# Optimization experiments

Measured on AMD Instinct MI355X. Metric: run time of the kernel, lower is better.

## Reference

```python
import jax, jax.numpy as jnp
import numpy as np

B, N, F, T = 8, 4096, 3, 12
D = 64            # model_dim
AH, DK, DV = 4, 32, 32   # attention headers, k_dim, v_dim
GH = 8            # gat_headers == out_features
E = 524288


def _ln(x, g, b, eps=1e-5):
    m = jnp.mean(x, -1, keepdims=True)
    v = jnp.mean((x - m) ** 2, -1, keepdims=True)
    return (x - m) * jax.lax.rsqrt(v + eps) * g + b


def _glu(x, w, b, C):
    # x: [B, C, N, L], w: [2C, C, 1, k] -> causal-style valid conv + SiLU gate
    y = jax.lax.conv_general_dilated(x, w, (1, 1), 'VALID',
                                     dimension_numbers=('NCHW', 'OIHW', 'NCHW'))
    y = y + b[None, :, None, None]
    return jax.nn.silu(y[:, :C]) * y[:, C:]


def setup_inputs():
    key = jax.random.key(0)
    ks = jax.random.split(key, 20)
    s = jnp.float32(0.02)
    return {
        'data': jax.random.normal(ks[0], (B, N, F, T), jnp.float32),
        'edges': jax.random.randint(ks[1], (2, E), 0, B * N),
        'embT_w': jax.random.normal(ks[2], (T, N)) * s,
        'embT_g': jnp.ones((N,)), 'embT_b': jnp.zeros((N,)),
        'wq': jax.random.normal(ks[3], (N, AH * DK)) * s,
        'wk': jax.random.normal(ks[4], (N, AH * DK)) * s,
        'wv': jax.random.normal(ks[5], (N, AH * DV)) * s,
        'wo': jax.random.normal(ks[6], (AH * DV, N)) * s,
        'tat_g': jnp.ones((N,)), 'tat_b': jnp.zeros((N,)),
        'mix_w': jax.random.normal(ks[7], (D, T, F)) * s,
        'mix_b': jnp.zeros((D,)),
        'embS_w': jax.random.normal(ks[8], (N, D)) * s,
        'embS_g': jnp.ones((D,)), 'embS_b': jnp.zeros((D,)),
        'gat_wl': jax.random.normal(ks[9], (D, GH * T)) * s,
        'gat_bl': jnp.zeros((GH * T,)),
        'gat_wr': jax.random.normal(ks[10], (D, GH * T)) * s,
        'gat_br': jnp.zeros((GH * T,)),
        'gat_att': jax.random.normal(ks[11], (GH, T)) * s,
        'gat_bias': jnp.zeros((GH * T,)),
        'g3_w': jax.random.normal(ks[12], (2 * GH, GH, 1, 3)) * s, 'g3_b': jnp.zeros((2 * GH,)),
        'g5_w': jax.random.normal(ks[13], (2 * GH, GH, 1, 5)) * s, 'g5_b': jnp.zeros((2 * GH,)),
        'g7_w': jax.random.normal(ks[14], (2 * GH, GH, 1, 7)) * s, 'g7_b': jnp.zeros((2 * GH,)),
        'fc_w': jax.random.normal(ks[15], (3 * T - 12, T)) * s, 'fc_b': jnp.zeros((T,)),
        'res_w': jax.random.normal(ks[16], (GH, F)) * s, 'res_b': jnp.zeros((GH,)),
        'ln_g': jnp.ones((GH,)), 'ln_b': jnp.zeros((GH,)),
    }


def reference(data, edges, embT_w, embT_g, embT_b, wq, wk, wv, wo, tat_g, tat_b,
              mix_w, mix_b, embS_w, embS_g, embS_b,
              gat_wl, gat_bl, gat_wr, gat_br, gat_att, gat_bias,
              g3_w, g3_b, g5_w, g5_b, g7_w, g7_b, fc_w, fc_b,
              res_w, res_b, ln_g, ln_b):
    # ---- EmbedT: [B,N,F,T] -> [B,F,T,N] plus learned temporal positional table
    x = data.transpose(0, 2, 3, 1) + embT_w[None, None]
    x = _ln(x, embT_g, embT_b)

    # ---- Temporal MHA over T (model_dim = N), dropout = identity in eval
    resid = x
    q = (x @ wq).reshape(B, F, T, AH, DK)
    k = (x @ wk).reshape(B, F, T, AH, DK)
    v = (x @ wv).reshape(B, F, T, AH, DV)
    scores = jnp.einsum('bfqhd,bfkhd->bfhqk', q, k) / jnp.sqrt(jnp.float32(DK))
    attn = jax.nn.softmax(scores, axis=-1)
    ctx = jnp.einsum('bfhqk,bfkhd->bfqhd', attn, v).reshape(B, F, T, AH * DV)
    x = _ln(ctx @ wo + resid, tat_g, tat_b)

    # ---- feature_temporal_mixer: Conv2d(T, D, (1, F)) on [B,T,N,F] -> [B,N,D]
    x = jnp.einsum('bftn,dtf->bnd', x, mix_w) + mix_b

    # ---- EmbedS
    x = _ln(x + embS_w[None], embS_g, embS_b)

    # ---- GATv2Conv over B*N nodes (add_self_loops=True, leaky slope 0.2)
    BN = B * N
    xf = x.reshape(BN, D)
    xl = (xf @ gat_wl + gat_bl).reshape(BN, GH, T)
    xr = (xf @ gat_wr + gat_br).reshape(BN, GH, T)
    loop = jnp.arange(BN)
    src = jnp.concatenate([edges[0], loop])
    dst = jnp.concatenate([edges[1], loop])
    feat = jax.nn.leaky_relu(xl[src] + xr[dst], 0.2)          # [E+BN, GH, T]
    e = jnp.einsum('eht,ht->eh', feat, gat_att)
    m = jax.ops.segment_max(e, dst, num_segments=BN)
    ex = jnp.exp(e - m[dst])
    ssum = jax.ops.segment_sum(ex, dst, num_segments=BN)
    alpha = ex / ssum[dst]
    out = jax.ops.segment_sum(xl[src] * alpha[:, :, None], dst, num_segments=BN)
    out = out.reshape(BN, GH * T) + gat_bias

    res_gate = out.reshape(B, N, GH, T).transpose(0, 2, 1, 3)  # [B,GH,N,T]

    # ---- gated convs (GLU) kernels 3/5/7 -> concat -> fc
    g = jnp.concatenate([_glu(res_gate, g3_w, g3_b, GH),
                         _glu(res_gate, g5_w, g5_b, GH),
                         _glu(res_gate, g7_w, g7_b, GH)], axis=-1)  # [B,GH,N,3T-12]
    x = jax.nn.relu(g @ fc_w + fc_b)   # features_num == 3 branch

    # ---- residual 1x1 conv over feature channels of raw data
    x_res = jnp.einsum('bfnt,of->bont', data.transpose(0, 2, 1, 3), res_w) \
            + res_b[None, :, None, None]
    x = jax.nn.relu(x_res + x)         # [B,GH,N,T]
    x = _ln(x.transpose(0, 3, 2, 1), ln_g, ln_b)  # LN over GH on [B,T,N,GH]
    return x.transpose(0, 2, 3, 1)     # [B,N,GH,T]
```

## Files before the change

### kernel.cpp

```cpp
#include <hip/hip_runtime.h>
#include <hip/hip_bf16.h>

typedef __hip_bfloat16 bf16;
typedef short bf16x8 __attribute__((ext_vector_type(8)));
typedef float f32x4 __attribute__((ext_vector_type(4)));
typedef unsigned short u16x4 __attribute__((ext_vector_type(4)));

constexpr int B = 8, N = 4096, F = 3, T = 12;
constexpr int Dm = 64, AH = 4, DK = 32;
constexpr int GH = 8;
constexpr int E = 524288;
constexpr int BN = B * N;
constexpr int ROWS = B * F * T;
constexpr int HD = AH * DK;
constexpr int PSZ = ROWS * 384;
constexpr int KSPLIT = 8;

__device__ __forceinline__ float b2f(bf16 x) { return __bfloat162float(x); }
__device__ __forceinline__ float u2f(unsigned short u) {
  return __uint_as_float(((unsigned)u) << 16);
}

constexpr unsigned C_EMBTW=0, C_EMBTG=49152, C_EMBTB=53248, C_WQ=57344,
  C_WK=581632, C_WV=1105920, C_WO=1630208, C_TATG=2154496, C_TATB=2158592,
  C_MIXW=2162688, C_MIXB=2164992, C_EMBSW=2165056, C_EMBSG=2427200,
  C_EMBSB=2427264, C_GWL=2427328, C_GBL=2433472, C_GWR=2433568,
  C_GBR=2439712, C_GATT=2439808, C_GBIAS=2439904, C_G3W=2440000,
  C_G3B=2440384, C_G5W=2440400, C_G5B=2441040, C_G7W=2441056,
  C_G7B=2441952, C_FCW=2441968, C_FCB=2442256, C_RW=2442268, C_RB=2442292,
  C_LNG=2442300, C_LNB=2442308, C_TOT=2442316;

__device__ const unsigned CUM[33] = {
  0,49152,53248,57344,581632,1105920,1630208,2154496,2158592,2162688,
  2164992,2165056,2427200,2427264,2427328,2433472,2433568,2439712,2439808,
  2439904,2440000,2440384,2440400,2441040,2441056,2441952,2441968,2442256,
  2442268,2442292,2442300,2442308,2442316};

constexpr size_t OFF_CVT = 16;
constexpr size_t OFF_X1  = OFF_CVT + 2442320;
constexpr size_t OFF_CTXB= OFF_X1  + (size_t)ROWS * N;
constexpr size_t OFF_X2  = OFF_CTXB+ (size_t)ROWS * HD;
constexpr size_t OFF_X3  = OFF_X2  + (size_t)ROWS * N;
constexpr size_t OFF_XL  = OFF_X3  + (size_t)BN * Dm;
constexpr size_t OFF_XR  = OFF_XL  + (size_t)BN * GH * T / 2;
constexpr size_t OFF_RG  = OFF_XR  + (size_t)BN * GH * T / 2;
constexpr size_t OFF_INT = OFF_RG  + (size_t)BN * GH * T;
constexpr size_t OFF_X2R = OFF_INT + 600000;
constexpr size_t OFF_WT16 = OFF_RG;
constexpr size_t OFF_WO16 = OFF_RG + 786432;
constexpr size_t OFF_X1B  = OFF_RG + 786432 + 262144;
constexpr size_t OFF_PP   = OFF_X1B + 294912;
constexpr size_t OFF_WOT  = OFF_PP + (size_t)KSPLIT * PSZ;
constexpr size_t OFF_GWT  = OFF_WOT + 262144;

struct Srcs { const void* p[32]; };
__global__ __launch_bounds__(256) void k_convert(
    const unsigned* __restrict__ g1, Srcs s, float* __restrict__ dst,
    bf16* __restrict__ wo16, int* __restrict__ cnt) {
  int f = (g1[0] != 0x3F800000u);
  for (unsigned gid = blockIdx.x * 256 + threadIdx.x;
       gid < C_TOT + 524288u + (unsigned)BN; gid += gridDim.x * 256) {
    if (gid < C_TOT) {
      int lo = 0, hi = 31;
      while (lo < hi) { int mid = (lo + hi + 1) >> 1; if (gid >= CUM[mid]) lo = mid; else hi = mid - 1; }
      if (lo >= 3 && lo <= 5) continue;
      unsigned off = gid - CUM[lo];
      dst[gid] = f ? b2f(((const bf16*)s.p[lo])[off]) : ((const float*)s.p[lo])[off];
    } else if (gid < C_TOT + 524288u) {
      unsigned off = gid - C_TOT;
      wo16[off] = f ? ((const bf16*)s.p[6])[off]
                    : __float2bfloat16(((const float*)s.p[6])[off]);
    } else {
      cnt[gid - C_TOT - 524288u] = 0;
    }
  }
}

__global__ __launch_bounds__(256) void k_wtrans(
    const unsigned* __restrict__ g1, const void* __restrict__ wq,
    const void* __restrict__ wk, const void* __restrict__ wv,
    bf16* __restrict__ wt) {
  __shared__ float t[32][33];
  int fl = (g1[0] != 0x3F800000u);
  int bid = blockIdx.x;
  int tc = bid / 128, tk = bid - tc * 128;
  int k0 = tk * 32, c0 = tc * 32;
  int mat = c0 >> 7, cloc = c0 & 127;
  const void* src = (mat == 0) ? wq : ((mat == 1) ? wk : wv);
  int tid = threadIdx.x;
  int r = tid >> 5, cc = tid & 31;
#pragma unroll
  for (int p = 0; p < 4; p++) {
    int row = p * 8 + r;
    size_t idx = (size_t)(k0 + row) * 128 + cloc + cc;
    t[row][cc] = fl ? b2f(((const bf16*)src)[idx]) : ((const float*)src)[idx];
  }
  __syncthreads();
#pragma unroll
  for (int p = 0; p < 4; p++) {
    int crow = p * 8 + r;
    wt[(size_t)(c0 + crow) * 4096 + k0 + cc] = __float2bfloat16(t[cc][crow]);
  }
}

__global__ __launch_bounds__(256) void k_wotrans(
    const bf16* __restrict__ wo, bf16* __restrict__ wot) {
  __shared__ bf16 t[32][33];
  int bid = blockIdx.x;
  int tn = bid >> 2, tk = bid & 3;
  int n0 = tn * 32, k0 = tk * 32;
  int tid = threadIdx.x;
  int r = tid >> 5, cc = tid & 31;
#pragma unroll
  for (int p = 0; p < 4; p++) {
    int row = p * 8 + r;
    t[row][cc] = wo[(size_t)(k0 + row) * 4096 + n0 + cc];
  }
  __syncthreads();
#pragma unroll
  for (int p = 0; p < 4; p++) {
    int crow = p * 8 + r;
    wot[(size_t)(n0 + crow) * 128 + k0 + cc] = t[cc][crow];
  }
}

__global__ __launch_bounds__(256) void k_gat_w(
    const float* __restrict__ wl, const float* __restrict__ wr,
    bf16* __restrict__ wlrt) {
  int idx = blockIdx.x * 256 + threadIdx.x;
  if (idx >= 192 * 64) return;
  int c = idx >> 6, k = idx & 63;
  float v = (c < 96) ? wl[(size_t)k * 96 + c] : wr[(size_t)k * 96 + (c - 96)];
  wlrt[idx] = __float2bfloat16(v);
}

__global__ __launch_bounds__(1024) void k_embt_ln(
    const unsigned* __restrict__ g1, const void* __restrict__ data,
    const float* __restrict__ w, const float* __restrict__ g,
    const float* __restrict__ b_, float* __restrict__ x1,
    bf16* __restrict__ x1b) {
  __shared__ float red[32];
  int row = blockIdx.x;
  int t = row % T; int bf_ = row / T; int f = bf_ % F; int bb = bf_ / F;
  int tid = threadIdx.x;
  int fl = (g1[0] != 0x3F800000u);
  float dv[4];
  if (fl) {
#pragma unroll
    for (int i = 0; i < 4; i++) {
      int n = i * 1024 + tid;
      dv[i] = b2f(((const bf16*)data)[(size_t)(bb * N + n) * 36 + f * 12 + t]);
    }
  } else {
#pragma unroll
    for (int i = 0; i < 4; i++) {
      int n = i * 1024 + tid;
      dv[i] = ((const float*)data)[(size_t)(bb * N + n) * 36 + f * 12 + t];
    }
  }
  float vals[4]; float s = 0.f, s2 = 0.f;
#pragma unroll
  for (int i = 0; i < 4; i++) {
    int n = i * 1024 + tid;
    float v = dv[i] + w[t * N + n];
    vals[i] = v; s += v; s2 += v * v;
  }
#pragma unroll
  for (int o = 32; o > 0; o >>= 1) { s += __shfl_down(s, o, 64); s2 += __shfl_down(s2, o, 64); }
  int lane = tid & 63, wid = tid >> 6;
  if (lane == 0) { red[wid] = s; red[16 + wid] = s2; }
  __syncthreads();
  float S = 0.f, S2 = 0.f;
#pragma unroll
  for (int j = 0; j < 16; j++) { S += red[j]; S2 += red[16 + j]; }
  float mean = S / (float)N;
  float var = S2 / (float)N - mean * mean;
  float inv = rsqrtf(var + 1e-5f);
#pragma unroll
  for (int i = 0; i < 4; i++) {
    int n = i * 1024 + tid;
    float o = (vals[i] - mean) * inv * g[n] + b_[n];
    x1[(size_t)row * N + n] = o;
    x1b[(size_t)row * N + n] = __float2bfloat16(o);
  }
}

__global__ __launch_bounds__(256) void k_qkv_mma(
    const bf16* __restrict__ x1b, const bf16* __restrict__ wt,
    float* __restrict__ pp) {
  int wave = (blockIdx.x * 256 + threadIdx.x) >> 6;
  int lane = threadIdx.x & 63;
  int ks = wave & 7, tile = wave >> 3;
  int mt = tile / 24, nt = tile - mt * 24;
  int m = lane & 15, quad = lane >> 4;
  const bf16* ap = x1b + (size_t)(mt * 16 + m) * 4096 + ks * 512 + quad * 8;
  const bf16* bp = wt  + (size_t)(nt * 16 + m) * 4096 + ks * 512 + quad * 8;
  f32x4 acc = {0.f, 0.f, 0.f, 0.f};
  for (int kk = 0; kk < 512; kk += 32) {
    bf16x8 a = *(const bf16x8*)(ap + kk);
    bf16x8 b = *(const bf16x8*)(bp + kk);
    acc = __builtin_amdgcn_mfma_f32_16x16x32_bf16(a, b, acc, 0, 0, 0);
  }
  float* o = pp + ((size_t)ks * ROWS + mt * 16 + quad * 4) * 384 + nt * 16 + m;
#pragma unroll
  for (int r = 0; r < 4; r++) o[(size_t)r * 384] = acc[r];
}

__global__ __launch_bounds__(64) void k_attn(
    const float* __restrict__ pp, bf16* __restrict__ ctxb) {
  int blk = blockIdx.x; int h = blk & 3; int bf_ = blk >> 2;
  int tid = threadIdx.x;
  __shared__ float qs[12][32], ks[12][32], vs[12][32], att[12][12];
  for (int idx = tid; idx < 384; idx += 64) {
    int t = idx >> 5, d = idx & 31;
    int base = (bf_ * T + t) * 384 + h * 32 + d;
    float qv = 0.f, kv = 0.f, vv = 0.f;
#pragma unroll
    for (int p = 0; p < KSPLIT; p++) {
      qv += pp[(size_t)p * PSZ + base];
      kv += pp[(size_t)p * PSZ + base + 128];
      vv += pp[(size_t)p * PSZ + base + 256];
    }
    qs[t][d] = qv; ks[t][d] = kv; vs[t][d] = vv;
  }
  __syncthreads();
  for (int idx = tid; idx < 144; idx += 64) {
    int qt = idx / 12, kt = idx - qt * 12;
    float s = 0.f;
#pragma unroll
    for (int d = 0; d < 32; d++) s += qs[qt][d] * ks[kt][d];
    att[qt][kt] = s * 0.1767766953f;
  }
  __syncthreads();
  if (tid < 12) {
    float m = -1e30f;
#pragma unroll
    for (int j = 0; j < 12; j++) m = fmaxf(m, att[tid][j]);
    float ss = 0.f;
#pragma unroll
    for (int j = 0; j < 12; j++) { float e = __expf(att[tid][j] - m); att[tid][j] = e; ss += e; }
    float inv = 1.f / ss;
#pragma unroll
    for (int j = 0; j < 12; j++) att[tid][j] *= inv;
  }
  __syncthreads();
  for (int idx = tid; idx < 384; idx += 64) {
    int t = idx >> 5, d = idx & 31;
    float s = 0.f;
#pragma unroll
    for (int j = 0; j < 12; j++) s += att[t][j] * vs[j][d];
    ctxb[(size_t)(bf_ * T + t) * HD + h * 32 + d] = __float2bfloat16(s);
  }
}

__global__ __launch_bounds__(256) void k_proj_mma(
    const bf16* __restrict__ ctxb, const bf16* __restrict__ wot,
    const float* __restrict__ x1, float* __restrict__ x2r) {
  int wave = (blockIdx.x * 256 + threadIdx.x) >> 6;
  int lane = threadIdx.x & 63;
  int nt = wave & 255, mt = wave >> 8;
  int m = lane & 15, quad = lane >> 4;
  const bf16* ap = ctxb + (size_t)(mt * 16 + m) * 128 + quad * 8;
  const bf16* bp = wot  + (size_t)(nt * 16 + m) * 128 + quad * 8;
  f32x4 acc = {0.f, 0.f, 0.f, 0.f};
#pragma unroll
  for (int kk = 0; kk < 128; kk += 32) {
    bf16x8 a = *(const bf16x8*)(ap + kk);
    bf16x8 b = *(const bf16x8*)(bp + kk);
    acc = __builtin_amdgcn_mfma_f32_16x16x32_bf16(a, b, acc, 0, 0, 0);
  }
  int row0 = mt * 16 + quad * 4, col = nt * 16 + m;
#pragma unroll
  for (int r = 0; r < 4; r++) {
    size_t idx = (size_t)(row0 + r) * N + col;
    x2r[idx] = acc[r] + x1[idx];
  }
}

__global__ __launch_bounds__(1024) void k_ln2(
    const float* __restrict__ x2r, const float* __restrict__ g,
    const float* __restrict__ b_, float* __restrict__ x2) {
  __shared__ float red[32];
  int row = blockIdx.x, tid = threadIdx.x;
  float vals[4]; float s = 0.f, s2 = 0.f;
#pragma unroll
  for (int i = 0; i < 4; i++) {
    int n = i * 1024 + tid;
    float v = x2r[(size_t)row * N + n];
    vals[i] = v; s += v; s2 += v * v;
  }
#pragma unroll
  for (int o = 32; o > 0; o >>= 1) { s += __shfl_down(s, o, 64); s2 += __shfl_down(s2, o, 64); }
  int lane = tid & 63, wid = tid >> 6;
  if (lane == 0) { red[wid] = s; red[16 + wid] = s2; }
  __syncthreads();
  float S = 0.f, S2 = 0.f;
#pragma unroll
  for (int j = 0; j < 16; j++) { S += red[j]; S2 += red[16 + j]; }
  float mean = S / (float)N;
  float var = S2 / (float)N - mean * mean;
  float inv = rsqrtf(var + 1e-5f);
#pragma unroll
  for (int i = 0; i < 4; i++) {
    int n = i * 1024 + tid;
    x2[(size_t)row * N + n] = (vals[i] - mean) * inv * g[n] + b_[n];
  }
}

__global__ __launch_bounds__(256) void k_mix_ln(
    const float* __restrict__ x2, const float* __restrict__ mw,
    const float* __restrict__ mb, const float* __restrict__ sw,
    const float* __restrict__ g, const float* __restrict__ b_,
    bf16* __restrict__ x3b) {
  int tid = threadIdx.x; int wid = tid >> 6; int d = tid & 63;
  int ng = blockIdx.x * 4 + wid;
  int bb = ng >> 12; int n = ng & (N - 1);
  float acc = mb[d];
#pragma unroll
  for (int t = 0; t < T; t++)
#pragma unroll
    for (int f = 0; f < F; f++)
      acc += x2[((size_t)(bb * F + f) * T + t) * N + n] * mw[(d * T + t) * F + f];
  acc += sw[(size_t)n * Dm + d];
  float s = acc, s2 = acc * acc;
#pragma unroll
  for (int m = 1; m < 64; m <<= 1) { s += __shfl_xor(s, m, 64); s2 += __shfl_xor(s2, m, 64); }
  float mean = s * (1.f / 64.f), var = s2 * (1.f / 64.f) - mean * mean;
  float inv = rsqrtf(var + 1e-5f);
  x3b[(size_t)ng * Dm + d] = __float2bfloat16((acc - mean) * inv * g[d] + b_[d]);
}

__global__ __launch_bounds__(256) void k_gat_mma(
    const bf16* __restrict__ x3b, const bf16* __restrict__ wlrt,
    const float* __restrict__ bl, const float* __restrict__ br,
    bf16* __restrict__ xl, bf16* __restrict__ xr) {
  __shared__ __align__(16) bf16 bs[192 * 64];
  int tid = threadIdx.x;
  {
    const bf16x8* src = (const bf16x8*)wlrt;
    bf16x8* dst = (bf16x8*)bs;
#pragma unroll
    for (int i = 0; i < 6; i++) {
      int ci = i * 256 + tid;
      dst[ci ^ ((ci >> 3) & 7)] = src[ci];
    }
  }
  __syncthreads();
  int wave = tid >> 6, lane = tid & 63;
  int mt = blockIdx.x * 4 + wave;
  int m = lane & 15, quad = lane >> 4;
  const bf16* ap = x3b + (size_t)(mt * 16 + m) * 64 + quad * 8;
  bf16x8 a0 = *(const bf16x8*)(ap);
  bf16x8 a1 = *(const bf16x8*)(ap + 32);
  const bf16x8* bs8 = (const bf16x8*)bs;
  int row0 = mt * 16 + quad * 4;
#pragma unroll
  for (int nt = 0; nt < 12; nt++) {
    int r = nt * 16 + m;
    int c0 = r * 8 + quad;
    bf16x8 b0 = bs8[c0 ^ (r & 7)];
    bf16x8 b1 = bs8[(c0 + 4) ^ (r & 7)];
    f32x4 acc = {0.f, 0.f, 0.f, 0.f};
    acc = __builtin_amdgcn_mfma_f32_16x16x32_bf16(a0, b0, acc, 0, 0, 0);
    acc = __builtin_amdgcn_mfma_f32_16x16x32_bf16(a1, b1, acc, 0, 0, 0);
    bool left = r < 96;
    int c = left ? r : r - 96;
    float bias = left ? bl[c] : br[c];
    bf16* o = left ? xl : xr;
#pragma unroll
    for (int rr = 0; rr < 4; rr++)
      o[(size_t)(row0 + rr) * 96 + c] = __float2bfloat16(acc[rr] + bias);
  }
}

__global__ __launch_bounds__(256) void k_hist(
    const int* __restrict__ edges, int* __restrict__ cnt) {
  int e = blockIdx.x * 256 + threadIdx.x;
  if (e < E) atomicAdd(cnt + edges[E + e], 1);
}

__global__ __launch_bounds__(1024) void k_scan(
    const int* __restrict__ cnt, int* __restrict__ off, int* __restrict__ cur) {
  __shared__ int part[1024];
  int tid = threadIdx.x;
  int base = tid * 32;
  int local[32]; int s = 0;
#pragma unroll
  for (int j = 0; j < 32; j++) { local[j] = cnt[base + j]; s += local[j]; }
  part[tid] = s;
  __syncthreads();
  for (int d = 1; d < 1024; d <<= 1) {
    int v = (tid >= d) ? part[tid - d] : 0;
    __syncthreads();
    part[tid] += v;
    __syncthreads();
  }
  int run = part[tid] - s;
#pragma unroll
  for (int j = 0; j < 32; j++) {
    off[base + j] = run; cur[base + j] = run;
    run += local[j];
  }
  if (tid == 1023) off[BN] = E;
}

__global__ __launch_bounds__(256) void k_scatter(
    const int* __restrict__ edges, int* __restrict__ cur, int* __restrict__ srcs) {
  int e = blockIdx.x * 256 + threadIdx.x;
  if (e < E) {
    int pos = atomicAdd(cur + edges[E + e], 1);
    srcs[pos] = edges[e];
  }
}

__device__ __forceinline__ void ld12bf(const bf16* p, float* l) {
  u16x4 a = *(const u16x4*)p;
  u16x4 b = *(const u16x4*)(p + 4);
  u16x4 c = *(const u16x4*)(p + 8);
  l[0]=u2f(a.x); l[1]=u2f(a.y); l[2]=u2f(a.z); l[3]=u2f(a.w);
  l[4]=u2f(b.x); l[5]=u2f(b.y); l[6]=u2f(b.z); l[7]=u2f(b.w);
  l[8]=u2f(c.x); l[9]=u2f(c.y); l[10]=u2f(c.z); l[11]=u2f(c.w);
}

__global__ __launch_bounds__(256) void k_gat(
    const int* __restrict__ off, const int* __restrict__ srcs,
    const bf16* __restrict__ xl, const bf16* __restrict__ xr,
    const float* __restrict__ att, const float* __restrict__ bias,
    float* __restrict__ rg) {
  int tid = threadIdx.x;
  int wv = tid >> 6, lane = tid & 63;
  int es = lane >> 3, h = lane & 7;
  int dst = blockIdx.x * 4 + wv;
  int bb = dst >> 12, n = dst & (N - 1);
  size_t rbase = (size_t)dst * 96 + h * 12;
  float xd[12], at[12];
  ld12bf(xr + rbase, xd);
#pragma unroll
  for (int t = 0; t < 12; t++) at[t] = att[h * 12 + t];

  float acc[12];
#pragma unroll
  for (int t = 0; t < 12; t++) acc[t] = 0.f;
  float ssum = 0.f;
  if (es == 0) {
    float l[12];
    ld12bf(xl + rbase, l);
    float sc = 0.f;
#pragma unroll
    for (int t = 0; t < 12; t++) {
      float sv = l[t] + xd[t];
      float fr = sv > 0.f ? sv : 0.2f * sv;
      sc += fr * at[t];
    }
    float ex = __expf(sc);
    ssum = ex;
#pragma unroll
    for (int t = 0; t < 12; t++) acc[t] = l[t] * ex;
  }
  int st = off[dst], en = off[dst + 1];
  for (int j = st + es; j < en; j += 8) {
    int src = srcs[j];
    float l[12];
    ld12bf(xl + (size_t)src * 96 + h * 12, l);
    float sc = 0.f;
#pragma unroll
    for (int t = 0; t < 12; t++) {
      float sv = l[t] + xd[t];
      float fr = sv > 0.f ? sv : 0.2f * sv;
      sc += fr * at[t];
    }
    float ex = __expf(sc);
    ssum += ex;
#pragma unroll
    for (int t = 0; t < 12; t++) acc[t] += l[t] * ex;
  }
#pragma unroll
  for (int m = 8; m < 64; m <<= 1) {
    ssum += __shfl_xor(ssum, m, 64);
#pragma unroll
    for (int t = 0; t < 12; t++) acc[t] += __shfl_xor(acc[t], m, 64);
  }
  if (es == 0) {
    float inv = 1.f / ssum;
    float* op = rg + ((size_t)(bb * 8 + h) * N + n) * 12;
#pragma unroll
    for (int t = 0; t < 12; t++)
      op[t] = acc[t] * inv + bias[h * 12 + t];
  }
}

__global__ __launch_bounds__(768) void k_tail(
    const unsigned* __restrict__ g1, const float* __restrict__ rg,
    const float* __restrict__ g3w, const float* __restrict__ g3b,
    const float* __restrict__ g5w, const float* __restrict__ g5b,
    const float* __restrict__ g7w, const float* __restrict__ g7b,
    const float* __restrict__ fcw, const float* __restrict__ fcb,
    const void* __restrict__ data, const float* __restrict__ rw,
    const float* __restrict__ rb, const float* __restrict__ lng,
    const float* __restrict__ lnb, void* __restrict__ out) {
  int tid = threadIdx.x;
  int br = tid >> 8;
  int u = tid & 255;
  int h = u & 7, i = u >> 3;
  int blk = blockIdx.x;
  int bb = blk >> 7;
  int n0 = (blk & 127) * 32;
  int n = n0 + i;
  int fl = (g1[0] != 0x3F800000u);
  __shared__ float xs[32][100];
  __shared__ float dds[32][40];
  __shared__ float wpk[8 * 260 + 4];
  __shared__ float fcs[288];
  __shared__ float gbuf[24][256];
  __shared__ float b3s[16], b5s[16], b7s[16], fcbs[12], lngs[8], lnbs[8], rws[24], rbs[8];
  for (int idx = tid; idx < 3072; idx += 768) {
    int c = idx / 384; int within = idx - c * 384;
    int ii = within / 12, t = within - ii * 12;
    xs[ii][c * 12 + t] = rg[((size_t)(bb * 8 + c) * N + n0 + ii) * 12 + t];
  }
  if (fl) {
    for (int idx = tid; idx < 1152; idx += 768) {
      int nn = idx / 36, jj = idx - nn * 36;
      dds[nn][jj] = b2f(((const bf16*)data)[(size_t)(bb * N + n0 + nn) * 36 + jj]);
    }
  } else {
    for (int idx = tid; idx < 1152; idx += 768) {
      int nn = idx / 36, jj = idx - nn * 36;
      dds[nn][jj] = ((const float*)data)[(size_t)(bb * N + n0 + nn) * 36 + jj];
    }
  }
  for (int idx = tid; idx < 1920; idx += 768) {
    int hh = idx / 240; int r = idx - hh * 240; int c = r / 30; int tap = r - c * 30;
    float v;
    if (tap < 3)       v = g3w[hh * 24 + c * 3 + tap];
    else if (tap < 6)  v = g3w[(hh + 8) * 24 + c * 3 + (tap - 3)];
    else if (tap < 11) v = g5w[hh * 40 + c * 5 + (tap - 6)];
    else if (tap < 16) v = g5w[(hh + 8) * 40 + c * 5 + (tap - 11)];
    else if (tap < 23) v = g7w[hh * 56 + c * 7 + (tap - 16)];
    else               v = g7w[(hh + 8) * 56 + c * 7 + (tap - 23)];
    wpk[hh * 260 + c * 32 + tap] = v;
  }
  for (int idx = tid; idx < 288; idx += 768) fcs[idx] = fcw[idx];
  if (tid < 16) { b3s[tid] = g3b[tid]; b5s[tid] = g5b[tid]; b7s[tid] = g7b[tid]; }
  if (tid < 12) fcbs[tid] = fcb[tid];
  if (tid < 24) rws[tid] = rw[tid];
  if (tid < 8) { lngs[tid] = lng[tid]; lnbs[tid] = lnb[tid]; rbs[tid] = rb[tid]; }
  __syncthreads();
  const float* x = xs[i];
  const float* wbase = &wpk[h * 260];
  if (br == 0) {
    float pa[10], pb[10];
    float ba = b3s[h], bbv = b3s[h + 8];
#pragma unroll
    for (int l = 0; l < 10; l++) { pa[l] = ba; pb[l] = bbv; }
#pragma unroll
    for (int c = 0; c < 8; c++) {
      float4 xa = *(const float4*)&x[c * 12];
      float4 xb = *(const float4*)&x[c * 12 + 4];
      float4 xc = *(const float4*)&x[c * 12 + 8];
      float xr[12] = {xa.x, xa.y, xa.z, xa.w, xb.x, xb.y, xb.z, xb.w,
                      xc.x, xc.y, xc.z, xc.w};
      const float* wpc = wbase + c * 32;
      float4 wA = *(const float4*)wpc;
      float2 wB = *(const float2*)(wpc + 4);
#pragma unroll
      for (int l = 0; l < 10; l++) {
        pa[l] += xr[l] * wA.x + xr[l + 1] * wA.y + xr[l + 2] * wA.z;
        pb[l] += xr[l] * wA.w + xr[l + 1] * wB.x + xr[l + 2] * wB.y;
      }
    }
#pragma unroll
    for (int l = 0; l < 10; l++)
      gbuf[l][u] = pa[l] / (1.f + __expf(-pa[l])) * pb[l];
  } else if (br == 1) {
    float pa[8], pb[8];
    float ba = b5s[h], bbv = b5s[h + 8];
#pragma unroll
    for (int l = 0; l < 8; l++) { pa[l] = ba; pb[l] = bbv; }
#pragma unroll
    for (int c = 0; c < 8; c++) {
      float4 xa = *(const float4*)&x[c * 12];
      float4 xb = *(const float4*)&x[c * 12 + 4];
      float4 xc = *(const float4*)&x[c * 12 + 8];
      float xr[12] = {xa.x, xa.y, xa.z, xa.w, xb.x, xb.y, xb.z, xb.w,
                      xc.x, xc.y, xc.z, xc.w};
      const float* wpc = wbase + c * 32;
      float2 w0 = *(const float2*)(wpc + 6);
      float2 w1 = *(const float2*)(wpc + 8);
      float2 w2 = *(const float2*)(wpc + 10);
      float2 w3 = *(const float2*)(wpc + 12);
      float2 w4 = *(const float2*)(wpc + 14);
      float wt[10] = {w0.x, w0.y, w1.x, w1.y, w2.x, w2.y, w3.x, w3.y, w4.x, w4.y};
#pragma unroll
      for (int l = 0; l < 8; l++) {
        float a = 0.f, bsum = 0.f;
#pragma unroll
        for (int j = 0; j < 5; j++) { a += xr[l + j] * wt[j]; bsum += xr[l + j] * wt[5 + j]; }
        pa[l] += a; pb[l] += bsum;
      }
    }
#pragma unroll
    for (int l = 0; l < 8; l++)
      gbuf[10 + l][u] = pa[l] / (1.f + __expf(-pa[l])) * pb[l];
  } else {
    float pa[6], pb[6];
    float ba = b7s[h], bbv = b7s[h + 8];
#pragma unroll
    for (int l = 0; l < 6; l++) { pa[l] = ba; pb[l] = bbv; }
#pragma unroll
    for (int c = 0; c < 8; c++) {
      float4 xa = *(const float4*)&x[c * 12];
      float4 xb = *(const float4*)&x[c * 12 + 4];
      float4 xc = *(const float4*)&x[c * 12 + 8];
      float xr[12] = {xa.x, xa.y, xa.z, xa.w, xb.x, xb.y, xb.z, xb.w,
                      xc.x, xc.y, xc.z, xc.w};
      const float* wpc = wbase + c * 32;
      float4 wA = *(const float4*)(wpc + 16);
      float4 wB = *(const float4*)(wpc + 20);
      float4 wC = *(const float4*)(wpc + 24);
      float2 wD = *(const float2*)(wpc + 28);
      float wt[14] = {wA.x, wA.y, wA.z, wA.w, wB.x, wB.y, wB.z, wB.w,
                      wC.x, wC.y, wC.z, wC.w, wD.x, wD.y};
#pragma unroll
      for (int l = 0; l < 6; l++) {
        float a = 0.f, bsum = 0.f;
#pragma unroll
        for (int j = 0; j < 7; j++) { a += xr[l + j] * wt[j]; bsum += xr[l + j] * wt[7 + j]; }
        pa[l] += a; pb[l] += bsum;
      }
    }
#pragma unroll
    for (int l = 0; l < 6; l++)
      gbuf[18 + l][u] = pa[l] / (1.f + __expf(-pa[l])) * pb[l];
  }
  __syncthreads();
  if (br == 0) {
    float gv[24];
#pragma unroll
    for (int l = 0; l < 24; l++) gv[l] = gbuf[l][u];
    float rw0 = rws[h * 3 + 0], rw1 = rws[h * 3 + 1], rw2 = rws[h * 3 + 2], rb0 = rbs[h];
    size_t obase = ((size_t)(bb * N + n) * GH + h) * T;
#pragma unroll
    for (int t = 0; t < 12; t++) {
      float a = fcbs[t];
#pragma unroll
      for (int l = 0; l < 24; l++) a += gv[l] * fcs[l * 12 + t];
      a = fmaxf(a, 0.f);
      float r = rb0 + dds[i][t] * rw0 + dds[i][12 + t] * rw1 + dds[i][24 + t] * rw2;
      float v = fmaxf(a + r, 0.f);
      float s = v, s2 = v * v;
#pragma unroll
      for (int m = 1; m < 8; m <<= 1) { s += __shfl_xor(s, m, 64); s2 += __shfl_xor(s2, m, 64); }
      float mean = s * 0.125f, var = s2 * 0.125f - mean * mean;
      float inv = rsqrtf(var + 1e-5f);
      float o = (v - mean) * inv * lngs[h] + lnbs[h];
      if (fl) ((bf16*)out)[obase + t] = __float2bfloat16(o);
      else    ((float*)out)[obase + t] = o;
    }
  }
}

extern "C" void kernel_launch(void* const* d_in, const int* in_sizes, int n_in,
                              void* d_out, int out_size, void* d_ws, size_t ws_size,
                              hipStream_t stream) {
  const void* data  = d_in[0];
  const int*  edges = (const int*)d_in[1];
  const unsigned* g1 = (const unsigned*)d_in[3];

  float* ws = (float*)d_ws;
  float* cv  = ws + OFF_CVT;
  float* x1  = ws + OFF_X1;  float* x2 = ws + OFF_X2;
  float* x2r = ws + OFF_X2R;
  bf16* x3b  = (bf16*)(ws + OFF_X3);
  bf16* ctxb = (bf16*)(ws + OFF_CTXB);
  bf16* xl   = (bf16*)(ws + OFF_XL);
  bf16* xr   = (bf16*)(ws + OFF_XR);
  float* rg  = ws + OFF_RG;
  bf16* wt16 = (bf16*)(ws + OFF_WT16);
  bf16* wo16 = (bf16*)(ws + OFF_WO16);
  bf16* x1b  = (bf16*)(ws + OFF_X1B);
  bf16* wot16= (bf16*)(ws + OFF_WOT);
  bf16* wlrt = (bf16*)(ws + OFF_GWT);
  float* pp  = ws + OFF_PP;
  int* ibase = (int*)(ws + OFF_INT);
  int* cnt  = ibase;
  int* off  = ibase + BN;
  int* srcs = ibase + 2 * BN + 16;

  Srcs s;
  for (int i = 0; i < 32; i++) s.p[i] = d_in[2 + i];

  k_convert<<<2048, 256, 0, stream>>>(g1, s, cv, wo16, cnt);
  k_wtrans<<<12 * 128, 256, 0, stream>>>(g1, d_in[5], d_in[6], d_in[7], wt16);
  k_wotrans<<<512, 256, 0, stream>>>(wo16, wot16);
  k_gat_w<<<48, 256, 0, stream>>>(cv + C_GWL, cv + C_GWR, wlrt);
  k_embt_ln<<<ROWS, 1024, 0, stream>>>(g1, data, cv + C_EMBTW, cv + C_EMBTG,
                                       cv + C_EMBTB, x1, x1b);
  k_qkv_mma<<<864, 256, 0, stream>>>(x1b, wt16, pp);
  k_attn<<<B * F * AH, 64, 0, stream>>>(pp, ctxb);
  k_proj_mma<<<1152, 256, 0, stream>>>(ctxb, wot16, x1, x2r);
  k_ln2<<<ROWS, 1024, 0, stream>>>(x2r, cv + C_TATG, cv + C_TATB, x2);
  k_mix_ln<<<BN / 4, 256, 0, stream>>>(x2, cv + C_MIXW, cv + C_MIXB, cv + C_EMBSW,
                                       cv + C_EMBSG, cv + C_EMBSB, x3b);
  k_gat_mma<<<512, 256, 0, stream>>>(x3b, wlrt, cv + C_GBL, cv + C_GBR, xl, xr);
  k_hist<<<E / 256, 256, 0, stream>>>(edges, cnt);
  k_scan<<<1, 1024, 0, stream>>>(cnt, off, cnt);
  k_scatter<<<E / 256, 256, 0, stream>>>(edges, cnt, srcs);
  k_gat<<<BN / 4, 256, 0, stream>>>(off, srcs, xl, xr, cv + C_GATT, cv + C_GBIAS, rg);
  k_tail<<<BN / 32, 768, 0, stream>>>(g1, rg, cv + C_G3W, cv + C_G3B, cv + C_G5W,
                                      cv + C_G5B, cv + C_G7W, cv + C_G7B, cv + C_FCW,
                                      cv + C_FCB, data, cv + C_RW, cv + C_RB,
                                      cv + C_LNG, cv + C_LNB, d_out);
}
```

Before: 352.3 us.

## Merge independent prep, histogram, scan and scatter kernels into fewer launches

```diff
diff --git a/kernel.cpp b/kernel.cpp
--- a/kernel.cpp
+++ b/kernel.cpp
@@ -19,6 +19,9 @@
 __device__ __forceinline__ float b2f(bf16 x) { return __bfloat162float(x); }
 __device__ __forceinline__ float u2f(unsigned short u) {
   return __uint_as_float(((unsigned)u) << 16);
+}
+__device__ __forceinline__ float ldf(const void* p, size_t i, int fl) {
+  return fl ? b2f(((const bf16*)p)[i]) : ((const float*)p)[i];
 }
 
 constexpr unsigned C_EMBTW=0, C_EMBTG=49152, C_EMBTB=53248, C_WQ=57344,
@@ -47,122 +50,110 @@
 constexpr size_t OFF_INT = OFF_RG  + (size_t)BN * GH * T;
 constexpr size_t OFF_X2R = OFF_INT + 600000;
 constexpr size_t OFF_WT16 = OFF_RG;
-constexpr size_t OFF_WO16 = OFF_RG + 786432;
 constexpr size_t OFF_X1B  = OFF_RG + 786432 + 262144;
 constexpr size_t OFF_PP   = OFF_X1B + 294912;
 constexpr size_t OFF_WOT  = OFF_PP + (size_t)KSPLIT * PSZ;
 constexpr size_t OFF_GWT  = OFF_WOT + 262144;
 
 struct Srcs { const void* p[32]; };
-__global__ __launch_bounds__(256) void k_convert(
-    const unsigned* __restrict__ g1, Srcs s, float* __restrict__ dst,
-    bf16* __restrict__ wo16, int* __restrict__ cnt) {
-  int f = (g1[0] != 0x3F800000u);
-  for (unsigned gid = blockIdx.x * 256 + threadIdx.x;
-       gid < C_TOT + 524288u + (unsigned)BN; gid += gridDim.x * 256) {
-    if (gid < C_TOT) {
-      int lo = 0, hi = 31;
-      while (lo < hi) { int mid = (lo + hi + 1) >> 1; if (gid >= CUM[mid]) lo = mid; else hi = mid - 1; }
-      if (lo >= 3 && lo <= 5) continue;
-      unsigned off = gid - CUM[lo];
-      dst[gid] = f ? b2f(((const bf16*)s.p[lo])[off]) : ((const float*)s.p[lo])[off];
-    } else if (gid < C_TOT + 524288u) {
-      unsigned off = gid - C_TOT;
-      wo16[off] = f ? ((const bf16*)s.p[6])[off]
-                    : __float2bfloat16(((const float*)s.p[6])[off]);
-    } else {
-      cnt[gid - C_TOT - 524288u] = 0;
-    }
-  }
-}
-
-__global__ __launch_bounds__(256) void k_wtrans(
-    const unsigned* __restrict__ g1, const void* __restrict__ wq,
-    const void* __restrict__ wk, const void* __restrict__ wv,
-    bf16* __restrict__ wt) {
-  __shared__ float t[32][33];
+
+__global__ __launch_bounds__(256) void k_prep(
+    const unsigned* __restrict__ g1, Srcs s, float* __restrict__ cv,
+    int* __restrict__ cnt, bf16* __restrict__ wt, bf16* __restrict__ wot,
+    bf16* __restrict__ wlrt) {
+  __shared__ float tf[32][33];
+  __shared__ bf16 tb[32][33];
   int fl = (g1[0] != 0x3F800000u);
-  int bid = blockIdx.x;
-  int tc = bid / 128, tk = bid - tc * 128;
-  int k0 = tk * 32, c0 = tc * 32;
-  int mat = c0 >> 7, cloc = c0 & 127;
-  const void* src = (mat == 0) ? wq : ((mat == 1) ? wk : wv);
+  int blk = blockIdx.x;
   int tid = threadIdx.x;
-  int r = tid >> 5, cc = tid & 31;
-#pragma unroll
-  for (int p = 0; p < 4; p++) {
-    int row = p * 8 + r;
-    size_t idx = (size_t)(k0 + row) * 128 + cloc + cc;
-    t[row][cc] = fl ? b2f(((const bf16*)src)[idx]) : ((const float*)src)[idx];
-  }
-  __syncthreads();
-#pragma unroll
-  for (int p = 0; p < 4; p++) {
-    int crow = p * 8 + r;
-    wt[(size_t)(c0 + crow) * 4096 + k0 + cc] = __float2bfloat16(t[cc][crow]);
-  }
-}
-
-__global__ __launch_bounds__(256) void k_wotrans(
-    const bf16* __restrict__ wo, bf16* __restrict__ wot) {
-  __shared__ bf16 t[32][33];
-  int bid = blockIdx.x;
-  int tn = bid >> 2, tk = bid & 3;
-  int n0 = tn * 32, k0 = tk * 32;
+  if (blk < 2048) {
+    for (unsigned gid = blk * 256 + tid; gid < C_TOT + (unsigned)BN;
+         gid += 2048 * 256) {
+      if (gid < C_TOT) {
+        int lo = 0, hi = 31;
+        while (lo < hi) { int mid = (lo + hi + 1) >> 1; if (gid >= CUM[mid]) lo = mid; else hi = mid - 1; }
+        if (lo >= 3 && lo <= 6) continue;
+        unsigned off = gid - CUM[lo];
+        cv[gid] = ldf(s.p[lo], off, fl);
+      } else {
+        cnt[gid - C_TOT] = 0;
+      }
+    }
+  } else if (blk < 3584) {
+    int bid = blk - 2048;
+    int tc = bid / 128, tk = bid - tc * 128;
+    int k0 = tk * 32, c0 = tc * 32;
+    int mat = c0 >> 7, cloc = c0 & 127;
+    const void* src = s.p[3 + mat];
+    int r = tid >> 5, cc = tid & 31;
+#pragma unroll
+    for (int p = 0; p < 4; p++) {
+      int row = p * 8 + r;
+      tf[row][cc] = ldf(src, (size_t)(k0 + row) * 128 + cloc + cc, fl);
+    }
+    __syncthreads();
+#pragma unroll
+    for (int p = 0; p < 4; p++) {
+      int crow = p * 8 + r;
+      wt[(size_t)(c0 + crow) * 4096 + k0 + cc] = __float2bfloat16(tf[cc][crow]);
+    }
+  } else if (blk < 4096) {
+    int bid = blk - 3584;
+    int tn = bid >> 2, tk = bid & 3;
+    int n0 = tn * 32, k0 = tk * 32;
+    const void* wo = s.p[6];
+    int r = tid >> 5, cc = tid & 31;
+#pragma unroll
+    for (int p = 0; p < 4; p++) {
+      int row = p * 8 + r;
+      size_t idx = (size_t)(k0 + row) * 4096 + n0 + cc;
+      tb[row][cc] = fl ? ((const bf16*)wo)[idx]
+                       : __float2bfloat16(((const float*)wo)[idx]);
+    }
+    __syncthreads();
+#pragma unroll
+    for (int p = 0; p < 4; p++) {
+      int crow = p * 8 + r;
+      wot[(size_t)(n0 + crow) * 128 + k0 + cc] = tb[cc][crow];
+    }
+  } else {
+    int idx = (blk - 4096) * 256 + tid;
+    if (idx < 192 * 64) {
+      int c = idx >> 6, k = idx & 63;
+      float v = (c < 96) ? ldf(s.p[14], (size_t)k * 96 + c, fl)
+                         : ldf(s.p[16], (size_t)k * 96 + (c - 96), fl);
+      wlrt[idx] = __float2bfloat16(v);
+    }
+  }
+}
+
+__global__ __launch_bounds__(1024) void k_embt_hist(
+    const unsigned* __restrict__ g1, const void* __restrict__ data,
+    const void* __restrict__ embw, const void* __restrict__ embg,
+    const void* __restrict__ embb, float* __restrict__ x1,
+    bf16* __restrict__ x1b, const int* __restrict__ edges,
+    int* __restrict__ cnt) {
+  __shared__ float red[32];
   int tid = threadIdx.x;
-  int r = tid >> 5, cc = tid & 31;
-#pragma unroll
-  for (int p = 0; p < 4; p++) {
-    int row = p * 8 + r;
-    t[row][cc] = wo[(size_t)(k0 + row) * 4096 + n0 + cc];
-  }
-  __syncthreads();
-#pragma unroll
-  for (int p = 0; p < 4; p++) {
-    int crow = p * 8 + r;
-    wot[(size_t)(n0 + crow) * 128 + k0 + cc] = t[cc][crow];
-  }
-}
-
-__global__ __launch_bounds__(256) void k_gat_w(
-    const float* __restrict__ wl, const float* __restrict__ wr,
-    bf16* __restrict__ wlrt) {
-  int idx = blockIdx.x * 256 + threadIdx.x;
-  if (idx >= 192 * 64) return;
-  int c = idx >> 6, k = idx & 63;
-  float v = (c < 96) ? wl[(size_t)k * 96 + c] : wr[(size_t)k * 96 + (c - 96)];
-  wlrt[idx] = __float2bfloat16(v);
-}
-
-__global__ __launch_bounds__(1024) void k_embt_ln(
-    const unsigned* __restrict__ g1, const void* __restrict__ data,
-    const float* __restrict__ w, const float* __restrict__ g,
-    const float* __restrict__ b_, float* __restrict__ x1,
-    bf16* __restrict__ x1b) {
-  __shared__ float red[32];
+  int fl = (g1[0] != 0x3F800000u);
+  if (blockIdx.x >= ROWS) {
+    int e = (blockIdx.x - ROWS) * 1024 + tid;
+    if (e < E) atomicAdd(cnt + edges[E + e], 1);
+    return;
+  }
   int row = blockIdx.x;
   int t = row % T; int bf_ = row / T; int f = bf_ % F; int bb = bf_ / F;
-  int tid = threadIdx.x;
-  int fl = (g1[0] != 0x3F800000u);
   float dv[4];
-  if (fl) {
-#pragma unroll
-    for (int i = 0; i < 4; i++) {
-      int n = i * 1024 + tid;
-      dv[i] = b2f(((const bf16*)data)[(size_t)(bb * N + n) * 36 + f * 12 + t]);
-    }
-  } else {
-#pragma unroll
-    for (int i = 0; i < 4; i++) {
-      int n = i * 1024 + tid;
-      dv[i] = ((const float*)data)[(size_t)(bb * N + n) * 36 + f * 12 + t];
-    }
-  }
-  float vals[4]; float s = 0.f, s2 = 0.f;
 #pragma unroll
   for (int i = 0; i < 4; i++) {
     int n = i * 1024 + tid;
-    float v = dv[i] + w[t * N + n];
+    dv[i] = ldf(data, (size_t)(bb * N + n) * 36 + f * 12 + t, fl);
+  }
+  float vals[4]; float s = 0.f, s2 = 0.f;
+#pragma unroll
+  for (int i = 0; i < 4; i++) {
+    int n = i * 1024 + tid;
+    float v = dv[i] + ldf(embw, (size_t)t * N + n, fl);
     vals[i] = v; s += v; s2 += v * v;
   }
 #pragma unroll
@@ -179,17 +170,41 @@
 #pragma unroll
   for (int i = 0; i < 4; i++) {
     int n = i * 1024 + tid;
-    float o = (vals[i] - mean) * inv * g[n] + b_[n];
+    float o = (vals[i] - mean) * inv * ldf(embg, n, fl) + ldf(embb, n, fl);
     x1[(size_t)row * N + n] = o;
     x1b[(size_t)row * N + n] = __float2bfloat16(o);
   }
 }
 
-__global__ __launch_bounds__(256) void k_qkv_mma(
+__global__ __launch_bounds__(256) void k_qkv_scan(
     const bf16* __restrict__ x1b, const bf16* __restrict__ wt,
-    float* __restrict__ pp) {
-  int wave = (blockIdx.x * 256 + threadIdx.x) >> 6;
-  int lane = threadIdx.x & 63;
+    float* __restrict__ pp, const int* __restrict__ cnt,
+    int* __restrict__ off, int* __restrict__ cur) {
+  __shared__ int part[256];
+  int tid = threadIdx.x;
+  if (blockIdx.x == 864) {
+    int base = tid * 128;
+    int s = 0;
+    for (int j = 0; j < 128; j++) s += cnt[base + j];
+    part[tid] = s;
+    __syncthreads();
+    for (int d = 1; d < 256; d <<= 1) {
+      int v = (tid >= d) ? part[tid - d] : 0;
+      __syncthreads();
+      part[tid] += v;
+      __syncthreads();
+    }
+    int run = part[tid] - s;
+    for (int j = 0; j < 128; j++) {
+      int c = cnt[base + j];
+      off[base + j] = run; cur[base + j] = run;
+      run += c;
+    }
+    if (tid == 255) off[BN] = E;
+    return;
+  }
+  int wave = (blockIdx.x * 256 + tid) >> 6;
+  int lane = tid & 63;
   int ks = wave & 7, tile = wave >> 3;
   int mt = tile / 24, nt = tile - mt * 24;
   int m = lane & 15, quad = lane >> 4;
@@ -206,11 +221,22 @@
   for (int r = 0; r < 4; r++) o[(size_t)r * 384] = acc[r];
 }
 
-__global__ __launch_bounds__(64) void k_attn(
-    const float* __restrict__ pp, bf16* __restrict__ ctxb) {
-  int blk = blockIdx.x; int h = blk & 3; int bf_ = blk >> 2;
-  int tid = threadIdx.x;
-  __shared__ float qs[12][32], ks[12][32], vs[12][32], att[12][12];
+__global__ __launch_bounds__(256) void k_attn_scatter(
+    const float* __restrict__ pp, bf16* __restrict__ ctxb,
+    const int* __restrict__ edges, int* __restrict__ cur,
+    int* __restrict__ srcs) {
+  if (blockIdx.x >= 24) {
+    int e = (blockIdx.x - 24) * 256 + threadIdx.x;
+    if (e < E) {
+      int pos = atomicAdd(cur + edges[E + e], 1);
+      srcs[pos] = edges[e];
+    }
+    return;
+  }
+  int bf_ = blockIdx.x;
+  int h = threadIdx.x >> 6;
+  int tid = threadIdx.x & 63;
+  __shared__ float qs[4][12][32], ks[4][12][32], vs[4][12][32], att[4][12][12];
   for (int idx = tid; idx < 384; idx += 64) {
     int t = idx >> 5, d = idx & 31;
     int base = (bf_ * T + t) * 384 + h * 32 + d;
@@ -221,34 +247,34 @@
       kv += pp[(size_t)p * PSZ + base + 128];
       vv += pp[(size_t)p * PSZ + base + 256];
     }
-    qs[t][d] = qv; ks[t][d] = kv; vs[t][d] = vv;
+    qs[h][t][d] = qv; ks[h][t][d] = kv; vs[h][t][d] = vv;
   }
   __syncthreads();
   for (int idx = tid; idx < 144; idx += 64) {
     int qt = idx / 12, kt = idx - qt * 12;
     float s = 0.f;
 #pragma unroll
-    for (int d = 0; d < 32; d++) s += qs[qt][d] * ks[kt][d];
-    att[qt][kt] = s * 0.1767766953f;
+    for (int d = 0; d < 32; d++) s += qs[h][qt][d] * ks[h][kt][d];
+    att[h][qt][kt] = s * 0.1767766953f;
   }
   __syncthreads();
   if (tid < 12) {
     float m = -1e30f;
 #pragma unroll
-    for (int j = 0; j < 12; j++) m = fmaxf(m, att[tid][j]);
+    for (int j = 0; j < 12; j++) m = fmaxf(m, att[h][tid][j]);
     float ss = 0.f;
 #pragma unroll
-    for (int j = 0; j < 12; j++) { float e = __expf(att[tid][j] - m); att[tid][j] = e; ss += e; }
+    for (int j = 0; j < 12; j++) { float e = __expf(att[h][tid][j] - m); att[h][tid][j] = e; ss += e; }
     float inv = 1.f / ss;
 #pragma unroll
-    for (int j = 0; j < 12; j++) att[tid][j] *= inv;
+    for (int j = 0; j < 12; j++) att[h][tid][j] *= inv;
   }
   __syncthreads();
   for (int idx = tid; idx < 384; idx += 64) {
     int t = idx >> 5, d = idx & 31;
     float s = 0.f;
 #pragma unroll
-    for (int j = 0; j < 12; j++) s += att[t][j] * vs[j][d];
+    for (int j = 0; j < 12; j++) s += att[h][t][j] * vs[h][j][d];
     ctxb[(size_t)(bf_ * T + t) * HD + h * 32 + d] = __float2bfloat16(s);
   }
 }
@@ -370,46 +396,6 @@
 #pragma unroll
     for (int rr = 0; rr < 4; rr++)
       o[(size_t)(row0 + rr) * 96 + c] = __float2bfloat16(acc[rr] + bias);
-  }
-}
-
-__global__ __launch_bounds__(256) void k_hist(
-    const int* __restrict__ edges, int* __restrict__ cnt) {
-  int e = blockIdx.x * 256 + threadIdx.x;
-  if (e < E) atomicAdd(cnt + edges[E + e], 1);
-}
-
-__global__ __launch_bounds__(1024) void k_scan(
-    const int* __restrict__ cnt, int* __restrict__ off, int* __restrict__ cur) {
-  __shared__ int part[1024];
-  int tid = threadIdx.x;
-  int base = tid * 32;
-  int local[32]; int s = 0;
-#pragma unroll
-  for (int j = 0; j < 32; j++) { local[j] = cnt[base + j]; s += local[j]; }
-  part[tid] = s;
-  __syncthreads();
-  for (int d = 1; d < 1024; d <<= 1) {
-    int v = (tid >= d) ? part[tid - d] : 0;
-    __syncthreads();
-    part[tid] += v;
-    __syncthreads();
-  }
-  int run = part[tid] - s;
-#pragma unroll
-  for (int j = 0; j < 32; j++) {
-    off[base + j] = run; cur[base + j] = run;
-    run += local[j];
-  }
-  if (tid == 1023) off[BN] = E;
-}
-
-__global__ __launch_bounds__(256) void k_scatter(
-    const int* __restrict__ edges, int* __restrict__ cur, int* __restrict__ srcs) {
-  int e = blockIdx.x * 256 + threadIdx.x;
-  if (e < E) {
-    int pos = atomicAdd(cur + edges[E + e], 1);
-    srcs[pos] = edges[e];
   }
 }
 
@@ -518,16 +504,9 @@
     int ii = within / 12, t = within - ii * 12;
     xs[ii][c * 12 + t] = rg[((size_t)(bb * 8 + c) * N + n0 + ii) * 12 + t];
   }
-  if (fl) {
-    for (int idx = tid; idx < 1152; idx += 768) {
-      int nn = idx / 36, jj = idx - nn * 36;
-      dds[nn][jj] = b2f(((const bf16*)data)[(size_t)(bb * N + n0 + nn) * 36 + jj]);
-    }
-  } else {
-    for (int idx = tid; idx < 1152; idx += 768) {
-      int nn = idx / 36, jj = idx - nn * 36;
-      dds[nn][jj] = ((const float*)data)[(size_t)(bb * N + n0 + nn) * 36 + jj];
-    }
+  for (int idx = tid; idx < 1152; idx += 768) {
+    int nn = idx / 36, jj = idx - nn * 36;
+    dds[nn][jj] = ldf(data, (size_t)(bb * N + n0 + nn) * 36 + jj, fl);
   }
   for (int idx = tid; idx < 1920; idx += 768) {
     int hh = idx / 240; int r = idx - hh * 240; int c = r / 30; int tap = r - c * 30;
@@ -677,7 +656,6 @@
   bf16* xr   = (bf16*)(ws + OFF_XR);
   float* rg  = ws + OFF_RG;
   bf16* wt16 = (bf16*)(ws + OFF_WT16);
-  bf16* wo16 = (bf16*)(ws + OFF_WO16);
   bf16* x1b  = (bf16*)(ws + OFF_X1B);
   bf16* wot16= (bf16*)(ws + OFF_WOT);
   bf16* wlrt = (bf16*)(ws + OFF_GWT);
@@ -690,22 +668,16 @@
   Srcs s;
   for (int i = 0; i < 32; i++) s.p[i] = d_in[2 + i];
 
-  k_convert<<<2048, 256, 0, stream>>>(g1, s, cv, wo16, cnt);
-  k_wtrans<<<12 * 128, 256, 0, stream>>>(g1, d_in[5], d_in[6], d_in[7], wt16);
-  k_wotrans<<<512, 256, 0, stream>>>(wo16, wot16);
-  k_gat_w<<<48, 256, 0, stream>>>(cv + C_GWL, cv + C_GWR, wlrt);
-  k_embt_ln<<<ROWS, 1024, 0, stream>>>(g1, data, cv + C_EMBTW, cv + C_EMBTG,
-                                       cv + C_EMBTB, x1, x1b);
-  k_qkv_mma<<<864, 256, 0, stream>>>(x1b, wt16, pp);
-  k_attn<<<B * F * AH, 64, 0, stream>>>(pp, ctxb);
+  k_prep<<<4144, 256, 0, stream>>>(g1, s, cv, cnt, wt16, wot16, wlrt);
+  k_embt_hist<<<ROWS + 512, 1024, 0, stream>>>(g1, data, d_in[2], d_in[3],
+                                               d_in[4], x1, x1b, edges, cnt);
+  k_qkv_scan<<<865, 256, 0, stream>>>(x1b, wt16, pp, cnt, off, cnt);
+  k_attn_scatter<<<24 + 2048, 256, 0, stream>>>(pp, ctxb, edges, cnt, srcs);
   k_proj_mma<<<1152, 256, 0, stream>>>(ctxb, wot16, x1, x2r);
   k_ln2<<<ROWS, 1024, 0, stream>>>(x2r, cv + C_TATG, cv + C_TATB, x2);
   k_mix_ln<<<BN / 4, 256, 0, stream>>>(x2, cv + C_MIXW, cv + C_MIXB, cv + C_EMBSW,
                                        cv + C_EMBSG, cv + C_EMBSB, x3b);
   k_gat_mma<<<512, 256, 0, stream>>>(x3b, wlrt, cv + C_GBL, cv + C_GBR, xl, xr);
-  k_hist<<<E / 256, 256, 0, stream>>>(edges, cnt);
-  k_scan<<<1, 1024, 0, stream>>>(cnt, off, cnt);
-  k_scatter<<<E / 256, 256, 0, stream>>>(edges, cnt, srcs);
   k_gat<<<BN / 4, 256, 0, stream>>>(off, srcs, xl, xr, cv + C_GATT, cv + C_GBIAS, rg);
   k_tail<<<BN / 32, 768, 0, stream>>>(g1, rg, cv + C_G3W, cv + C_G3B, cv + C_G5W,
                                       cv + C_G5B, cv + C_G7W, cv + C_G7B, cv + C_FCW,
```

Measured after the change: 331.2 us. 6.0% less time.
